# Optimization experiments

Measured on AMD Instinct MI355X. Metric: run time of the kernel, lower is better.

## Reference

```python
import jax, jax.numpy as jnp
import numpy as np

L, B, T = 2048, 2048, 7


def setup_inputs() -> dict:
    key = jax.random.key(0)
    k = jax.random.split(key, 6)
    emissions = jax.random.normal(k[0], (L, B, T), dtype=jnp.float32)
    tags = jax.random.randint(k[1], (L, B), 0, T, dtype=jnp.int32)
    qmask = jnp.zeros((L, B), dtype=jnp.int32)   # single speaker per conversation
    mask = jnp.ones((L, B), dtype=jnp.int32)     # first timestep must be all-on
    u = lambda kk, shp: jax.random.uniform(kk, shp, jnp.float32, -0.1, 0.1)
    return {
        'emissions': emissions, 'tags': tags, 'qmask': qmask, 'mask': mask,
        'start_transitions': u(k[2], (T,)),
        'end_transitions': u(k[3], (T,)),
        'self_transitions': u(k[4], (T, T)),
        'other_transitions': u(k[5], (T, T)),
    }


def _crf_llh(emissions, tags, qmask, mask, start_transitions, end_transitions,
             self_transitions, other_transitions):
    # emissions: [L, B, T]; tags/qmask/mask: [L, B]
    Lx, Bx, Tx = emissions.shape
    maskf = mask.astype(emissions.dtype)
    # contagion[i]: utterance i follows an utterance by a different speaker
    contagion = qmask[1:] != qmask[:-1]                                  # [L-1, B]
    brange = jnp.arange(Bx)

    # ---- numerator: score of the gold tag path (CRF._compute_score) ----
    em_tag = jnp.take_along_axis(emissions, tags[:, :, None], axis=2)[:, :, 0]   # [L, B]
    trans_tag = jnp.where(contagion,
                          other_transitions[tags[:-1], tags[1:]],
                          self_transitions[tags[:-1], tags[1:]])                 # [L-1, B]
    score = start_transitions[tags[0]] + em_tag[0]
    score = score + jnp.sum((trans_tag + em_tag[1:]) * maskf[1:], axis=0)
    seq_ends = mask.sum(axis=0) - 1                                              # [B]
    score = score + end_transitions[tags[seq_ends, brange]]

    # ---- denominator: partition function via sequential log-sum-exp scan ----
    def step(alpha, xs):
        em_i, cont_i, m_i = xs
        trans = jnp.where(cont_i[:, None, None],
                          other_transitions[None], self_transitions[None])       # [B, T, T]
        new = jax.nn.logsumexp(alpha[:, :, None] + trans, axis=1) + em_i         # [B, T]
        alpha = jnp.where(m_i[:, None] > 0, new, alpha)
        return alpha, None

    alpha0 = start_transitions[None, :] + emissions[0]                           # [B, T]
    alpha, _ = jax.lax.scan(step, alpha0, (emissions[1:], contagion, mask[1:]))
    logZ = jax.nn.logsumexp(alpha + end_transitions[None, :], axis=1)            # [B]

    return jnp.sum(score - logZ)   # reduction='sum'


def reference(emissions, tags, qmask, mask, start_transitions, end_transitions,
              self_transitions, other_transitions):
    return _crf_llh(emissions, tags, qmask, mask, start_transitions,
                    end_transitions, self_transitions, other_transitions)
```

## Files before the change

### kernel.cpp

```cpp
#include <hip/hip_runtime.h>
#include <hip/hip_bf16.h>

#define LSEQ 2048
#define BB   2048
#define TT   7
#define NFLD 17

typedef float f4 __attribute__((ext_vector_type(4)));

__device__ __forceinline__ void ld7(const float* __restrict__ p, float* e) {
  f4 lo, hi;
  __builtin_memcpy(&lo, p, 16);
  __builtin_memcpy(&hi, p + 3, 16);
  e[0] = lo.x; e[1] = lo.y; e[2] = lo.z; e[3] = lo.w;
  e[4] = hi.y; e[5] = hi.z; e[6] = hi.w;
}

template<int KCH>
__global__ __launch_bounds__(256)
void crf_chunk_kernel(const float* __restrict__ em,
                      const int*   __restrict__ tags,
                      const int*   __restrict__ qmask,
                      const int*   __restrict__ mask,
                      const float* __restrict__ self_t,
                      const float* __restrict__ other_t,
                      float* __restrict__ recs) {
  constexpr int CC  = LSEQ / KCH;
  constexpr int NG  = KCH * BB;
  constexpr int NGH = NG / 2;
  constexpr int NB  = 12;
  __shared__ float sE[2][49];
  __shared__ float sT[2][49];
  int tid = threadIdx.x;
  if (tid < 49) {
    float sv = self_t[tid], ov = other_t[tid];
    sE[0][tid] = __expf(sv); sE[1][tid] = __expf(ov);
    sT[0][tid] = sv;         sT[1][tid] = ov;
  }
  __syncthreads();

  int role = tid >> 7;
  int p = blockIdx.x * 128 + (tid & 127);
  int b  = p & (BB - 1);
  int c1 = p >> 11;
  int c2 = c1 + KCH / 2;
  int g1 = p, g2 = p + NGH;

  float Es[49];
  int loadedCont = -1;
  auto loadEs = [&](int cf) {
#pragma unroll
    for (int k = 0; k < 49; ++k)
      Es[k] = __int_as_float(
          __builtin_amdgcn_readfirstlane(__float_as_int(sE[cf][k])));
    loadedCont = cf;
  };

  if (role == 0) {
    float vA[7], vB[7];
#pragma unroll
    for (int t = 0; t < 7; ++t) { vA[t] = 1.f; vB[t] = 1.f; }
    float scA = 0.f, scB = 0.f, LvA = 0.f, LvB = 0.f;
    int mcA = 0, mcB = 0, tpA, qpA, tpB, qpB;
    int iA = c1 * CC, iB = c2 * CC;
    if (c1 == 0) { mcA = mask[b]; tpA = tags[b]; qpA = qmask[b]; }
    else { size_t pb = (size_t)(iA - 1) * BB + b; tpA = tags[pb]; qpA = qmask[pb]; }
    { size_t pb = (size_t)(iB - 1) * BB + b; tpB = tags[pb]; qpB = qmask[pb]; }

    auto LDA = [&](int s, float* e, int& tg, int& qm, int& mi) {
      size_t base = (size_t)(iA + s) * BB + b;
      ld7(em + base * TT, e);
      tg = tags[base]; qm = qmask[base]; mi = mask[base];
    };
    auto LDB = [&](int s, float* e, int& tg, int& qm, int& mi) {
      size_t base = (size_t)(iB + s) * BB + b;
      ld7(em + base * TT, e);
      tg = tags[base]; qm = qmask[base]; mi = mask[base];
    };

    auto STEP = [&](const float* e, int tg, int qm, int mi,
                    float* v, float& sc, int& mc, int& tp, int& qp) {
      int cont = (qm != qp) ? 1 : 0;
      int cf = __builtin_amdgcn_readfirstlane(cont);
      bool uni = __all(cont == cf);
      float ee[7];
#pragma unroll
      for (int t = 0; t < 7; ++t) ee[t] = __expf(e[t]);
      float etag = e[0];
#pragma unroll
      for (int t = 1; t < 7; ++t) etag = (tg == t) ? e[t] : etag;
      float ttag = sT[cont][tp * 7 + tg];
      if (mi) { sc += ttag + etag; ++mc; }
      tp = tg; qp = qm;
      float a[7] = {0.f,0.f,0.f,0.f,0.f,0.f,0.f};
      if (uni) {
        if (cf != loadedCont) loadEs(cf);
#pragma unroll
        for (int r = 0; r < 7; ++r) {
          float vr = v[r];
#pragma unroll
          for (int t = 0; t < 7; ++t) a[t] = fmaf(vr, Es[r*7+t], a[t]);
        }
      } else {
        loadedCont = -1;
#pragma unroll
        for (int r = 0; r < 7; ++r) {
          float vr = v[r];
#pragma unroll
          for (int t = 0; t < 7; ++t) a[t] = fmaf(vr, sE[cont][r*7+t], a[t]);
        }
      }
#pragma unroll
      for (int t = 0; t < 7; ++t) v[t] = mi ? a[t] * ee[t] : v[t];
    };

    float eA0[7], eA1[7], eB0[7], eB1[7];
    int tgA0, qmA0, miA0, tgA1, qmA1, miA1;
    int tgB0, qmB0, miB0, tgB1, qmB1, miB1;
    LDA(0, eA0, tgA0, qmA0, miA0);
    LDB(0, eB0, tgB0, qmB0, miB0);

    for (int j = 0; j < CC; ++j) {
      bool more = (j + 1 < CC);
      if (more) {
        LDA(j + 1, eA1, tgA1, qmA1, miA1);
        LDB(j + 1, eB1, tgB1, qmB1, miB1);
      }
      int miA = (c1 == 0 && j == 0) ? 0 : miA0;
      STEP(eA0, tgA0, qmA0, miA, vA, scA, mcA, tpA, qpA);
      STEP(eB0, tgB0, qmB0, miB0, vB, scB, mcB, tpB, qpB);
      if ((j & 7) == 7) {
        float sA = vA[0]+vA[1]+vA[2]+vA[3]+vA[4]+vA[5]+vA[6];
        float sB = vB[0]+vB[1]+vB[2]+vB[3]+vB[4]+vB[5]+vB[6];
        LvA += logf(sA); LvB += logf(sB);
        float iA2 = 1.0f / sA, iB2 = 1.0f / sB;
#pragma unroll
        for (int t = 0; t < 7; ++t) { vA[t] *= iA2; vB[t] *= iB2; }
      }
      if (more) {
#pragma unroll
        for (int t = 0; t < 7; ++t) { eA0[t] = eA1[t]; eB0[t] = eB1[t]; }
        tgA0 = tgA1; qmA0 = qmA1; miA0 = miA1;
        tgB0 = tgB1; qmB0 = qmB1; miB0 = miB1;
      }
    }
    float sA = vA[0]+vA[1]+vA[2]+vA[3]+vA[4]+vA[5]+vA[6];
    float sB = vB[0]+vB[1]+vB[2]+vB[3]+vB[4]+vB[5]+vB[6];
    float iA2 = 1.0f / sA, iB2 = 1.0f / sB;
#pragma unroll
    for (int t = 0; t < 7; ++t) {
      recs[(size_t)t * NG + g1] = vA[t] * iA2;
      recs[(size_t)t * NG + g2] = vB[t] * iB2;
    }
    recs[(size_t)14 * NG + g1] = scA;
    recs[(size_t)14 * NG + g2] = scB;
    recs[(size_t)15 * NG + g1] = (float)mcA;
    recs[(size_t)15 * NG + g2] = (float)mcB;
    recs[(size_t)16 * NG + g1] = LvA + logf(sA);
    recs[(size_t)16 * NG + g2] = LvB + logf(sB);
  } else {
    float rA[7], rB[7];
#pragma unroll
    for (int t = 0; t < 7; ++t) { rA[t] = 1.f; rB[t] = 1.f; }
    int iloA = (c1 == 0) ? 1 : c1 * CC;
    int iloB = c2 * CC;

    auto LDbA = [&](int s, float* e, int& q, int& q1, int& mi) {
      size_t base = (size_t)(iloA + NB - 1 - s) * BB + b;
      ld7(em + base * TT, e);
      q = qmask[base]; q1 = qmask[base - BB]; mi = mask[base];
    };
    auto LDbB = [&](int s, float* e, int& q, int& q1, int& mi) {
      size_t base = (size_t)(iloB + NB - 1 - s) * BB + b;
      ld7(em + base * TT, e);
      q = qmask[base]; q1 = qmask[base - BB]; mi = mask[base];
    };

    auto STEPB = [&](const float* e, int q, int q1, int mi, float* r) {
      int cont = (q != q1) ? 1 : 0;
      int cf = __builtin_amdgcn_readfirstlane(cont);
      bool uni = __all(cont == cf);
      float ee[7];
#pragma unroll
      for (int t = 0; t < 7; ++t) ee[t] = __expf(e[t]);
      float tmp[7];
#pragma unroll
      for (int t = 0; t < 7; ++t) tmp[t] = ee[t] * r[t];
      float a[7] = {0.f,0.f,0.f,0.f,0.f,0.f,0.f};
      if (uni) {
        if (cf != loadedCont) loadEs(cf);
#pragma unroll
        for (int t = 0; t < 7; ++t) {
          float tt = tmp[t];
#pragma unroll
          for (int s2 = 0; s2 < 7; ++s2) a[s2] = fmaf(tt, Es[s2*7+t], a[s2]);
        }
      } else {
        loadedCont = -1;
#pragma unroll
        for (int t = 0; t < 7; ++t) {
          float tt = tmp[t];
#pragma unroll
          for (int s2 = 0; s2 < 7; ++s2) a[s2] = fmaf(tt, sE[cont][s2*7+t], a[s2]);
        }
      }
#pragma unroll
      for (int s2 = 0; s2 < 7; ++s2) r[s2] = mi ? a[s2] : r[s2];
    };

    float eA0[7], eA1[7], eB0[7], eB1[7];
    int qA0, q1A0, mA0, qA1, q1A1, mA1;
    int qB0, q1B0, mB0, qB1, q1B1, mB1;
    LDbA(0, eA0, qA0, q1A0, mA0);
    LDbB(0, eB0, qB0, q1B0, mB0);

    for (int j = 0; j < NB; ++j) {
      bool more = (j + 1 < NB);
      if (more) {
        LDbA(j + 1, eA1, qA1, q1A1, mA1);
        LDbB(j + 1, eB1, qB1, q1B1, mB1);
      }
      STEPB(eA0, qA0, q1A0, mA0, rA);
      STEPB(eB0, qB0, q1B0, mB0, rB);
      if (j == 5) {
        float sA = rA[0]+rA[1]+rA[2]+rA[3]+rA[4]+rA[5]+rA[6];
        float sB = rB[0]+rB[1]+rB[2]+rB[3]+rB[4]+rB[5]+rB[6];
        float iA2 = 1.0f / sA, iB2 = 1.0f / sB;
#pragma unroll
        for (int t = 0; t < 7; ++t) { rA[t] *= iA2; rB[t] *= iB2; }
      }
      if (more) {
#pragma unroll
        for (int t = 0; t < 7; ++t) { eA0[t] = eA1[t]; eB0[t] = eB1[t]; }
        qA0 = qA1; q1A0 = q1A1; mA0 = mA1;
        qB0 = qB1; q1B0 = q1B1; mB0 = mB1;
      }
    }
    float sA = rA[0]+rA[1]+rA[2]+rA[3]+rA[4]+rA[5]+rA[6];
    float sB = rB[0]+rB[1]+rB[2]+rB[3]+rB[4]+rB[5]+rB[6];
    float iA2 = 1.0f / sA, iB2 = 1.0f / sB;
#pragma unroll
    for (int t = 0; t < 7; ++t) {
      recs[(size_t)(7 + t) * NG + g1] = rA[t] * iA2;
      recs[(size_t)(7 + t) * NG + g2] = rB[t] * iB2;
    }
  }
}

template<int KCH>
__global__ __launch_bounds__(256)
void crf_junction_kernel(const float* __restrict__ recs,
                         const float* __restrict__ em,
                         const int*   __restrict__ tags,
                         const float* __restrict__ start_t,
                         const float* __restrict__ end_t,
                         float* __restrict__ partials) {
  constexpr int NG = KCH * BB;
  int tid = threadIdx.x;
  int g = blockIdx.x * 256 + tid;
  int b = g & (BB - 1);
  int c = g >> 11;
  float rn[7];
#pragma unroll
  for (int t = 0; t < 7; ++t) rn[t] = recs[(size_t)(7 + t) * NG + g];
  float term = recs[(size_t)14 * NG + g] - recs[(size_t)16 * NG + g];
  float dot = 0.f;
  if (c == 0) {
    float e0[7], st[7];
#pragma unroll
    for (int t = 0; t < 7; ++t) { e0[t] = em[(size_t)b * TT + t]; st[t] = start_t[t]; }
#pragma unroll
    for (int t = 0; t < 7; ++t) dot = fmaf(__expf(st[t] + e0[t]), rn[t], dot);
    int tg0 = tags[b];
    float em0t = e0[0], stt = st[0];
#pragma unroll
    for (int t = 1; t < 7; ++t) {
      em0t = (tg0 == t) ? e0[t] : em0t;
      stt  = (tg0 == t) ? st[t] : stt;
    }
    term += stt + em0t;
  } else {
#pragma unroll
    for (int t = 0; t < 7; ++t)
      dot = fmaf(recs[(size_t)t * NG + (g - BB)], rn[t], dot);
  }
  term -= logf(dot);
  if (c == KCH - 1) {
    float fz = 0.f;
#pragma unroll
    for (int t = 0; t < 7; ++t)
      fz = fmaf(recs[(size_t)t * NG + g], __expf(end_t[t]), fz);
    term -= logf(fz);
    float mcf = 0.f;
    for (int cc = 0; cc < KCH; ++cc)
      mcf += recs[(size_t)15 * NG + (size_t)cc * BB + b];
    int se = (int)mcf - 1;
    int te = tags[(size_t)se * BB + b];
    term += end_t[te];
  }
  __shared__ float red[256];
  red[tid] = term;
  __syncthreads();
  for (int off = 128; off > 0; off >>= 1) {
    if (tid < off) red[tid] += red[tid + off];
    __syncthreads();
  }
  if (tid == 0) partials[blockIdx.x] = red[0];
}

__global__ __launch_bounds__(1024)
void crf_reduce_kernel(const float* __restrict__ partials, int n,
                       float* __restrict__ out) {
  __shared__ float s[1024];
  int t = threadIdx.x;
  float v = 0.f;
  for (int i = t; i < n; i += 1024) v += partials[i];
  s[t] = v;
  __syncthreads();
  for (int off = 512; off > 0; off >>= 1) {
    if (t < off) s[t] += s[t + off];
    __syncthreads();
  }
  if (t == 0) out[0] = s[0];
}

extern "C" void kernel_launch(void* const* d_in, const int* in_sizes, int n_in,
                              void* d_out, int out_size, void* d_ws, size_t ws_size,
                              hipStream_t stream) {
  const float* em      = (const float*)d_in[0];
  const int*   tags    = (const int*)d_in[1];
  const int*   qmask   = (const int*)d_in[2];
  const int*   mask    = (const int*)d_in[3];
  const float* start_t = (const float*)d_in[4];
  const float* end_t   = (const float*)d_in[5];
  const float* self_t  = (const float*)d_in[6];
  const float* other_t = (const float*)d_in[7];

  float* recs = (float*)d_ws;

  constexpr int KCH = 64;
  constexpr int NG  = KCH * BB;
  float* partials = recs + (size_t)NFLD * NG;

  crf_chunk_kernel<KCH><<<(NG / 2) / 128, 256, 0, stream>>>(
      em, tags, qmask, mask, self_t, other_t, recs);
  crf_junction_kernel<KCH><<<NG / 256, 256, 0, stream>>>(
      recs, em, tags, start_t, end_t, partials);
  crf_reduce_kernel<<<1, 1024, 0, stream>>>(partials, NG / 256, (float*)d_out);
}
```

Baseline: 52.66 us.

## Split forward and backward chunk work into separate blocks with LDS-staged emission tiles

Forward-scan threads now run in their own blocks, one chunk chain per thread instead of two interleaved chains. Each wave stages its emission rows into a double-buffered shared-memory tile with aligned 16-byte loads, replacing the unaligned 7-float per-thread loads. Backward-role threads move to a separate set of blocks in the same launch. The aim is fewer, better-formed memory transactions and more parallel blocks. The cost is less per-thread ILP and about 57KB of LDS per block, which limits occupancy.

```diff
diff --git a/kernel.cpp b/kernel.cpp
--- a/kernel.cpp
+++ b/kernel.cpp
@@ -25,12 +25,17 @@
                       const float* __restrict__ self_t,
                       const float* __restrict__ other_t,
                       float* __restrict__ recs) {
-  constexpr int CC  = LSEQ / KCH;
-  constexpr int NG  = KCH * BB;
-  constexpr int NGH = NG / 2;
-  constexpr int NB  = 12;
+  constexpr int CC   = LSEQ / KCH;
+  constexpr int NG   = KCH * BB;
+  constexpr int NGH  = NG / 2;
+  constexpr int NB   = 12;
+  constexpr int NT   = CC / 4;
+  constexpr int NFWD = NG / 256;
+
   __shared__ float sE[2][49];
   __shared__ float sT[2][49];
+  __shared__ float sTileF[2][4 * 256 * TT];
+
   int tid = threadIdx.x;
   if (tid < 49) {
     float sv = self_t[tid], ov = other_t[tid];
@@ -39,13 +44,6 @@
   }
   __syncthreads();
 
-  int role = tid >> 7;
-  int p = blockIdx.x * 128 + (tid & 127);
-  int b  = p & (BB - 1);
-  int c1 = p >> 11;
-  int c2 = c1 + KCH / 2;
-  int g1 = p, g2 = p + NGH;
-
   float Es[49];
   int loadedCont = -1;
   auto loadEs = [&](int cf) {
@@ -56,127 +54,148 @@
     loadedCont = cf;
   };
 
-  if (role == 0) {
-    float vA[7], vB[7];
-#pragma unroll
-    for (int t = 0; t < 7; ++t) { vA[t] = 1.f; vB[t] = 1.f; }
-    float scA = 0.f, scB = 0.f, LvA = 0.f, LvB = 0.f;
-    int mcA = 0, mcB = 0, tpA, qpA, tpB, qpB;
-    int iA = c1 * CC, iB = c2 * CC;
-    if (c1 == 0) { mcA = mask[b]; tpA = tags[b]; qpA = qmask[b]; }
-    else { size_t pb = (size_t)(iA - 1) * BB + b; tpA = tags[pb]; qpA = qmask[pb]; }
-    { size_t pb = (size_t)(iB - 1) * BB + b; tpB = tags[pb]; qpB = qmask[pb]; }
-
-    auto LDA = [&](int s, float* e, int& tg, int& qm, int& mi) {
-      size_t base = (size_t)(iA + s) * BB + b;
-      ld7(em + base * TT, e);
-      tg = tags[base]; qm = qmask[base]; mi = mask[base];
-    };
-    auto LDB = [&](int s, float* e, int& tg, int& qm, int& mi) {
-      size_t base = (size_t)(iB + s) * BB + b;
-      ld7(em + base * TT, e);
-      tg = tags[base]; qm = qmask[base]; mi = mask[base];
-    };
-
-    auto STEP = [&](const float* e, int tg, int qm, int mi,
-                    float* v, float& sc, int& mc, int& tp, int& qp) {
-      int cont = (qm != qp) ? 1 : 0;
-      int cf = __builtin_amdgcn_readfirstlane(cont);
-      bool uni = __all(cont == cf);
-      float ee[7];
-#pragma unroll
-      for (int t = 0; t < 7; ++t) ee[t] = __expf(e[t]);
-      float etag = e[0];
-#pragma unroll
-      for (int t = 1; t < 7; ++t) etag = (tg == t) ? e[t] : etag;
-      float ttag = sT[cont][tp * 7 + tg];
-      if (mi) { sc += ttag + etag; ++mc; }
-      tp = tg; qp = qm;
-      float a[7] = {0.f,0.f,0.f,0.f,0.f,0.f,0.f};
-      if (uni) {
-        if (cf != loadedCont) loadEs(cf);
-#pragma unroll
-        for (int r = 0; r < 7; ++r) {
-          float vr = v[r];
-#pragma unroll
-          for (int t = 0; t < 7; ++t) a[t] = fmaf(vr, Es[r*7+t], a[t]);
+  int bid = blockIdx.x;
+  if (bid < NFWD) {
+    int lane = tid & 63, wv = tid >> 6;
+    int g = bid * 256 + tid;
+    int b = g & (BB - 1);
+    int b0 = (bid * 256) & (BB - 1);
+    int c = g >> 11;
+    int i_base = c * CC;
+
+    float v[7] = {1.f,1.f,1.f,1.f,1.f,1.f,1.f};
+    float sc = 0.f, Lv = 0.f;
+    int mc = 0, tp, qp;
+    if (c == 0) { mc = mask[b]; tp = tags[b]; qp = qmask[b]; }
+    else { size_t pb = (size_t)(i_base - 1) * BB + b; tp = tags[pb]; qp = qmask[pb]; }
+
+    auto LOADT = [&](int k, f4* rg) {
+#pragma unroll
+      for (int r = 0; r < 7; ++r) {
+        int slot = r * 64 + lane;
+        int row = slot / 112, wi = slot - row * 112;
+        const float* p = em + ((size_t)(i_base + k * 4 + row) * BB
+                               + (size_t)b0 + (size_t)wv * 64) * TT;
+        __builtin_memcpy(&rg[r], p + wi * 4, 16);
+      }
+    };
+    auto WRITET = [&](int bf, const f4* rg) {
+#pragma unroll
+      for (int r = 0; r < 7; ++r) {
+        int slot = r * 64 + lane;
+        int row = slot / 112, wi = slot - row * 112;
+        __builtin_memcpy(&sTileF[bf][(row * 448 + wv * 112 + wi) * 4], &rg[r], 16);
+      }
+    };
+    auto LDFLAGS = [&](int k, int* tg, int* qm, int* mi) {
+#pragma unroll
+      for (int s = 0; s < 4; ++s) {
+        size_t base = (size_t)(i_base + k * 4 + s) * BB + b;
+        tg[s] = tags[base]; qm[s] = qmask[base]; mi[s] = mask[base];
+      }
+    };
+
+    f4 rg[7];
+    LOADT(0, rg); WRITET(0, rg);
+    int tg[4], qm[4], mi[4];
+    LDFLAGS(0, tg, qm, mi);
+    int buf = 0;
+
+    for (int k = 0; k < NT; ++k) {
+      bool more = (k + 1 < NT);
+      if (more) LOADT(k + 1, rg);
+      int tgn[4], qmn[4], min_[4];
+      if (more) LDFLAGS(k + 1, tgn, qmn, min_);
+
+      const float* lb = sTileF[buf];
+#pragma unroll
+      for (int s = 0; s < 4; ++s) {
+        const float* e = lb + s * 1792 + wv * 448 + lane * 7;
+        int m = (c == 0 && k == 0 && s == 0) ? 0 : mi[s];
+
+        int cont = (qm[s] != qp) ? 1 : 0;
+        int cf = __builtin_amdgcn_readfirstlane(cont);
+        bool uni = __all(cont == cf);
+        float ee[7];
+#pragma unroll
+        for (int t = 0; t < 7; ++t) ee[t] = __expf(e[t]);
+        float etag = e[0];
+#pragma unroll
+        for (int t = 1; t < 7; ++t) etag = (tg[s] == t) ? e[t] : etag;
+        float ttag = sT[cont][tp * 7 + tg[s]];
+        if (m) { sc += ttag + etag; ++mc; }
+        tp = tg[s]; qp = qm[s];
+
+        float a[7] = {0.f,0.f,0.f,0.f,0.f,0.f,0.f};
+        if (uni) {
+          if (cf != loadedCont) loadEs(cf);
+#pragma unroll
+          for (int r = 0; r < 7; ++r) {
+            float vr = v[r];
+#pragma unroll
+            for (int t = 0; t < 7; ++t) a[t] = fmaf(vr, Es[r*7+t], a[t]);
+          }
+        } else {
+          loadedCont = -1;
+#pragma unroll
+          for (int r = 0; r < 7; ++r) {
+            float vr = v[r];
+#pragma unroll
+            for (int t = 0; t < 7; ++t) a[t] = fmaf(vr, sE[cont][r*7+t], a[t]);
+          }
         }
-      } else {
-        loadedCont = -1;
-#pragma unroll
-        for (int r = 0; r < 7; ++r) {
-          float vr = v[r];
-#pragma unroll
-          for (int t = 0; t < 7; ++t) a[t] = fmaf(vr, sE[cont][r*7+t], a[t]);
-        }
-      }
-#pragma unroll
-      for (int t = 0; t < 7; ++t) v[t] = mi ? a[t] * ee[t] : v[t];
-    };
-
-    float eA0[7], eA1[7], eB0[7], eB1[7];
-    int tgA0, qmA0, miA0, tgA1, qmA1, miA1;
-    int tgB0, qmB0, miB0, tgB1, qmB1, miB1;
-    LDA(0, eA0, tgA0, qmA0, miA0);
-    LDB(0, eB0, tgB0, qmB0, miB0);
-
-    for (int j = 0; j < CC; ++j) {
-      bool more = (j + 1 < CC);
+#pragma unroll
+        for (int t = 0; t < 7; ++t) v[t] = m ? a[t] * ee[t] : v[t];
+      }
+
+      if (k & 1) {
+        float ss = v[0]+v[1]+v[2]+v[3]+v[4]+v[5]+v[6];
+        Lv += logf(ss);
+        float inv = 1.0f / ss;
+#pragma unroll
+        for (int t = 0; t < 7; ++t) v[t] *= inv;
+      }
+
       if (more) {
-        LDA(j + 1, eA1, tgA1, qmA1, miA1);
-        LDB(j + 1, eB1, tgB1, qmB1, miB1);
-      }
-      int miA = (c1 == 0 && j == 0) ? 0 : miA0;
-      STEP(eA0, tgA0, qmA0, miA, vA, scA, mcA, tpA, qpA);
-      STEP(eB0, tgB0, qmB0, miB0, vB, scB, mcB, tpB, qpB);
-      if ((j & 7) == 7) {
-        float sA = vA[0]+vA[1]+vA[2]+vA[3]+vA[4]+vA[5]+vA[6];
-        float sB = vB[0]+vB[1]+vB[2]+vB[3]+vB[4]+vB[5]+vB[6];
-        LvA += logf(sA); LvB += logf(sB);
-        float iA2 = 1.0f / sA, iB2 = 1.0f / sB;
-#pragma unroll
-        for (int t = 0; t < 7; ++t) { vA[t] *= iA2; vB[t] *= iB2; }
-      }
-      if (more) {
-#pragma unroll
-        for (int t = 0; t < 7; ++t) { eA0[t] = eA1[t]; eB0[t] = eB1[t]; }
-        tgA0 = tgA1; qmA0 = qmA1; miA0 = miA1;
-        tgB0 = tgB1; qmB0 = qmB1; miB0 = miB1;
-      }
+        WRITET(buf ^ 1, rg);
+#pragma unroll
+        for (int s = 0; s < 4; ++s) { tg[s]=tgn[s]; qm[s]=qmn[s]; mi[s]=min_[s]; }
+      }
+      buf ^= 1;
     }
-    float sA = vA[0]+vA[1]+vA[2]+vA[3]+vA[4]+vA[5]+vA[6];
-    float sB = vB[0]+vB[1]+vB[2]+vB[3]+vB[4]+vB[5]+vB[6];
-    float iA2 = 1.0f / sA, iB2 = 1.0f / sB;
-#pragma unroll
-    for (int t = 0; t < 7; ++t) {
-      recs[(size_t)t * NG + g1] = vA[t] * iA2;
-      recs[(size_t)t * NG + g2] = vB[t] * iB2;
-    }
-    recs[(size_t)14 * NG + g1] = scA;
-    recs[(size_t)14 * NG + g2] = scB;
-    recs[(size_t)15 * NG + g1] = (float)mcA;
-    recs[(size_t)15 * NG + g2] = (float)mcB;
-    recs[(size_t)16 * NG + g1] = LvA + logf(sA);
-    recs[(size_t)16 * NG + g2] = LvB + logf(sB);
+
+    float ss = v[0]+v[1]+v[2]+v[3]+v[4]+v[5]+v[6];
+    float inv = 1.0f / ss;
+#pragma unroll
+    for (int t = 0; t < 7; ++t) recs[(size_t)t * NG + g] = v[t] * inv;
+    recs[(size_t)14 * NG + g] = sc;
+    recs[(size_t)15 * NG + g] = (float)mc;
+    recs[(size_t)16 * NG + g] = Lv + logf(ss);
   } else {
+    int p = (bid - NFWD) * 256 + tid;
+    int b  = p & (BB - 1);
+    int c1 = p >> 11;
+    int c2 = c1 + KCH / 2;
+    int g1 = p, g2 = p + NGH;
+
     float rA[7], rB[7];
 #pragma unroll
     for (int t = 0; t < 7; ++t) { rA[t] = 1.f; rB[t] = 1.f; }
     int iloA = (c1 == 0) ? 1 : c1 * CC;
     int iloB = c2 * CC;
 
-    auto LDbA = [&](int s, float* e, int& q, int& q1, int& mi) {
+    auto LDbA = [&](int s, float* e, int& q, int& q1, int& mi2) {
       size_t base = (size_t)(iloA + NB - 1 - s) * BB + b;
       ld7(em + base * TT, e);
-      q = qmask[base]; q1 = qmask[base - BB]; mi = mask[base];
-    };
-    auto LDbB = [&](int s, float* e, int& q, int& q1, int& mi) {
+      q = qmask[base]; q1 = qmask[base - BB]; mi2 = mask[base];
+    };
+    auto LDbB = [&](int s, float* e, int& q, int& q1, int& mi2) {
       size_t base = (size_t)(iloB + NB - 1 - s) * BB + b;
       ld7(em + base * TT, e);
-      q = qmask[base]; q1 = qmask[base - BB]; mi = mask[base];
-    };
-
-    auto STEPB = [&](const float* e, int q, int q1, int mi, float* r) {
+      q = qmask[base]; q1 = qmask[base - BB]; mi2 = mask[base];
+    };
+
+    auto STEPB = [&](const float* e, int q, int q1, int mi2, float* r) {
       int cont = (q != q1) ? 1 : 0;
       int cf = __builtin_amdgcn_readfirstlane(cont);
       bool uni = __all(cont == cf);
@@ -205,7 +224,7 @@
         }
       }
 #pragma unroll
-      for (int s2 = 0; s2 < 7; ++s2) r[s2] = mi ? a[s2] : r[s2];
+      for (int s2 = 0; s2 < 7; ++s2) r[s2] = mi2 ? a[s2] : r[s2];
     };
 
     float eA0[7], eA1[7], eB0[7], eB1[7];
@@ -342,7 +361,9 @@
   constexpr int NG  = KCH * BB;
   float* partials = recs + (size_t)NFLD * NG;
 
-  crf_chunk_kernel<KCH><<<(NG / 2) / 128, 256, 0, stream>>>(
+  int fwd_blocks = NG / 256;
+  int bwd_blocks = (NG / 2) / 256;
+  crf_chunk_kernel<KCH><<<fwd_blocks + bwd_blocks, 256, 0, stream>>>(
       em, tags, qmask, mask, self_t, other_t, recs);
   crf_junction_kernel<KCH><<<NG / 256, 256, 0, stream>>>(
       recs, em, tags, start_t, end_t, partials);
```

Result: slower. 72.10 us (+36.9%).
